# Kernel tuning notes

Measured on AMD Instinct MI355X. Metric: run time of the kernel, lower is better.

## Reference

```python
import jax, jax.numpy as jnp
import numpy as np

H = 32          # num_heads
DN = 128        # qk_nope_head_dim
DR = 64         # qk_rope_head_dim
DV = 128        # v_head_dim
HID = 4096      # hidden_size
QR = 1536       # q_lora_rank
KVR = 512       # kv_lora_rank
EPS = 1e-6
MAXP = 4096     # max_position_embeddings


def _rope_tables():
    inv_freq = 1.0 / (10000.0 ** (np.arange(0, DR, 2, dtype=np.float32) / DR))
    t = np.arange(MAXP, dtype=np.float32)
    freqs = np.outer(t, inv_freq)
    emb = np.concatenate([freqs, freqs], axis=-1)  # [MAXP, DR]
    return jnp.asarray(np.cos(emb), jnp.float32), jnp.asarray(np.sin(emb), jnp.float32)


def _rotate_half(x):
    x1, x2 = x[..., : x.shape[-1] // 2], x[..., x.shape[-1] // 2 :]
    return jnp.concatenate([-x2, x1], axis=-1)


def _rms_norm(x, w, eps=EPS):
    var = jnp.mean(jnp.square(x), axis=-1, keepdims=True)
    return x * jax.lax.rsqrt(var + eps) * w


def setup_inputs() -> dict:
    key = jax.random.key(0)
    ks = jax.random.split(key, 9)
    s = 0.02
    return {
        "hidden_states": jax.random.normal(ks[0], (2, 2048, HID), jnp.float32),
        "position_ids": jnp.arange(2 * 2048, dtype=jnp.int64).reshape(2, 2048) % MAXP,
        "q_a_w": jax.random.normal(ks[1], (QR, HID), jnp.float32) * s,
        "q_a_ln_w": jnp.ones((QR,), jnp.float32),
        "q_b_w": jax.random.normal(ks[2], (H * (DN + DR), QR), jnp.float32) * s,
        "kv_a_w": jax.random.normal(ks[3], (KVR, HID), jnp.float32) * s,
        "kv_a_ln_w": jnp.ones((KVR,), jnp.float32),
        "kv_b_w": jax.random.normal(ks[4], (H * (DN + DV), KVR), jnp.float32) * s,
        "k_rope_w": jax.random.normal(ks[5], (H * DR, HID), jnp.float32) * s,
        "o_w": jax.random.normal(ks[6], (HID, H * DV), jnp.float32) * s,
    }


def reference(hidden_states, position_ids, q_a_w, q_a_ln_w, q_b_w,
              kv_a_w, kv_a_ln_w, kv_b_w, k_rope_w, o_w):
    bsz, q_len, _ = hidden_states.shape
    cos_tab, sin_tab = _rope_tables()

    # Q low-rank path
    q = hidden_states @ q_a_w.T                      # [B,S,QR]
    q = _rms_norm(q, q_a_ln_w)
    q = q @ q_b_w.T                                  # [B,S,H*(DN+DR)]
    q = q.reshape(bsz, q_len, H, DN + DR).transpose(0, 2, 1, 3)  # [B,H,S,DN+DR]
    q_nope, q_rope = q[..., :DN], q[..., DN:]

    # KV low-rank path
    kv = _rms_norm(hidden_states @ kv_a_w.T, kv_a_ln_w)          # [B,S,KVR]
    kv = (kv @ kv_b_w.T).reshape(bsz, q_len, H, DN + DV).transpose(0, 2, 1, 3)
    k_nope, v = kv[..., :DN], kv[..., DN:]                        # [B,H,S,DN],[B,H,S,DV]

    k_rope = (hidden_states @ k_rope_w.T).reshape(bsz, q_len, H, DR).transpose(0, 2, 1, 3)

    # decoupled RoPE
    cos = cos_tab[position_ids][:, None, :, :]       # [B,1,S,DR]
    sin = sin_tab[position_ids][:, None, :, :]
    q_rope = q_rope * cos + _rotate_half(q_rope) * sin
    k_rope = k_rope * cos + _rotate_half(k_rope) * sin

    full_q = jnp.concatenate([q_nope, q_rope], axis=-1)  # [B,H,S,DN+DR]
    full_k = jnp.concatenate([k_nope, k_rope], axis=-1)

    scale = 1.0 / jnp.sqrt(jnp.float32(DN + DR))
    attn = jnp.einsum("bhqd,bhkd->bhqk", full_q, full_k) * scale
    attn = jax.nn.softmax(attn.astype(jnp.float32), axis=-1).astype(full_q.dtype)
    out = jnp.einsum("bhqk,bhkd->bhqd", attn, v)          # [B,H,S,DV]
    out = out.transpose(0, 2, 1, 3).reshape(bsz, q_len, H * DV)
    return out @ o_w.T                                     # [B,S,HID]
```

## Files before the change

kernel.cpp:

```cpp
#include <hip/hip_runtime.h>
#include <hip/hip_bf16.h>
#include <math.h>


typedef __attribute__((ext_vector_type(8))) short s16x8;
typedef __attribute__((ext_vector_type(4))) float f32x4;
typedef __attribute__((ext_vector_type(4))) unsigned short u16x4;

#define DEV __device__ __forceinline__

constexpr int Bc = 2, Sc = 2048, Tc = Bc * Sc;
constexpr int Hc = 32, DNc = 128, DRc = 64, DVc = 128;
constexpr int HIDc = 4096, QRc = 1536, KVRc = 512;
constexpr int DQK = DNc + DRc;

DEV unsigned short f2bf(float f) {
  unsigned u = __float_as_uint(f);
  return (unsigned short)((u + 0x7fffu + ((u >> 16) & 1u)) >> 16);
}
DEV float bf2f(unsigned short u) { return __uint_as_float(((unsigned)u) << 16); }

DEV void gll16(const void* g, void* l) {
  __builtin_amdgcn_global_load_lds((const __attribute__((address_space(1))) void*)g,
                                   (__attribute__((address_space(3))) void*)l, 16, 0, 0);
}
DEV f32x4 mfma_bf16(s16x8 a, s16x8 b, f32x4 c) {
  return __builtin_amdgcn_mfma_f32_16x16x32_bf16(a, b, c, 0, 0, 0);
}
DEV unsigned cvt_pk_bf16(float a, float b) {
  unsigned r;
  asm("v_cvt_pk_bf16_f32 %0, %1, %2" : "=v"(r) : "v"(a), "v"(b));
  return r;
}

__global__ __launch_bounds__(256) void cast_k(const float* __restrict__ in,
                                              unsigned short* __restrict__ out, long n) {
  long i = ((long)blockIdx.x * 256 + threadIdx.x) * 4;
  if (i >= n) return;
  float4 v = *(const float4*)(in + i);
  u16x4 o;
  o.x = f2bf(v.x); o.y = f2bf(v.y); o.z = f2bf(v.z); o.w = f2bf(v.w);
  *(u16x4*)(out + i) = o;
}

template <int COLS>
__global__ __launch_bounds__(256) void rmsnorm_bf_k(unsigned short* __restrict__ x,
                                                    const float* __restrict__ w,
                                                    int pitch) {
  const int row = blockIdx.x;
  unsigned short* p = x + (size_t)row * pitch;
  float ss = 0.f;
  for (int c = threadIdx.x * 8; c < COLS; c += 2048) {
    s16x8 v = *(const s16x8*)&p[c];
    #pragma unroll
    for (int j = 0; j < 8; ++j) { const float f = bf2f((unsigned short)v[j]); ss += f * f; }
  }
  #pragma unroll
  for (int off = 1; off < 64; off <<= 1) ss += __shfl_xor(ss, off, 64);
  __shared__ float sred[4];
  if ((threadIdx.x & 63) == 0) sred[threadIdx.x >> 6] = ss;
  __syncthreads();
  const float inv = rsqrtf((sred[0] + sred[1] + sred[2] + sred[3]) / (float)COLS + 1e-6f);
  for (int c = threadIdx.x * 8; c < COLS; c += 2048) {
    s16x8 v = *(const s16x8*)&p[c];
    s16x8 o;
    #pragma unroll
    for (int j = 0; j < 8; ++j)
      o[j] = (short)f2bf(bf2f((unsigned short)v[j]) * inv * w[c + j]);
    *(s16x8*)&p[c] = o;
  }
}

template <bool OUTF32>
__global__ __launch_bounds__(512, 2) void gemm256_bt(const unsigned short* __restrict__ A,
                                                     int lda,
                                                     const unsigned short* __restrict__ B,
                                                     void* __restrict__ Cout,
                                                     int M, int N, int K) {
  __shared__ unsigned short As[2][256 * 64];
  __shared__ unsigned short Bs[2][256 * 64];
  const int tid = threadIdx.x;
  const int wv = tid >> 6, l = tid & 63;
  const int lo = l & 15, hi = l >> 4;
  const int wm = wv >> 2, wn = wv & 3;
  const int nbx = N >> 8;
  const int nwg = (M >> 8) * nbx;
  const int orig = blockIdx.x;
  const int q8 = nwg >> 3, r8 = nwg & 7, xc = orig & 7, o8 = orig >> 3;
  const int wg = (xc < r8 ? xc * (q8 + 1) : r8 * (q8 + 1) + (xc - r8) * q8) + o8;
  const int bx = wg % nbx, by = wg / nbx;
  const int m0 = by * 256, n0 = bx * 256;
  const int lrow = l >> 3;
  const int lcol = (((l & 7) ^ lrow) << 3);

  f32x4 acc[8][4] = {};
  const int NKT = K >> 6;

  auto stage = [&](int bi, int kt) {
    #pragma unroll
    for (int i = 0; i < 4; ++i) {
      const int r0 = wv * 32 + i * 8;
      gll16(A + (size_t)(m0 + r0 + lrow) * lda + kt + lcol, (void*)&As[bi][r0 * 64]);
    }
    #pragma unroll
    for (int i = 0; i < 4; ++i) {
      const int r0 = wv * 32 + i * 8;
      gll16(B + (size_t)(n0 + r0 + lrow) * K + kt + lcol, (void*)&Bs[bi][r0 * 64]);
    }
  };

  stage(0, 0);

  for (int t = 0; t < NKT; ++t) {
    const int bi = t & 1;
    if (t + 1 < NKT) stage(bi ^ 1, (t + 1) * 64);
    __builtin_amdgcn_sched_barrier(0);
    if (t + 1 < NKT) asm volatile("s_waitcnt vmcnt(8)" ::: "memory");
    else             asm volatile("s_waitcnt vmcnt(0)" ::: "memory");
    __builtin_amdgcn_s_barrier();
    __builtin_amdgcn_sched_barrier(0);

    const unsigned short* Ab = As[bi];
    const unsigned short* Bb = Bs[bi];
    auto rdA = [&](int m, int kk) -> s16x8 {
      const int row = wm * 128 + m * 16 + lo;
      return *(const s16x8*)&Ab[row * 64 + ((kk * 32 + hi * 8) ^ ((row & 7) << 3))];
    };
    auto rdB = [&](int n, int kk) -> s16x8 {
      const int row = wn * 64 + n * 16 + lo;
      return *(const s16x8*)&Bb[row * 64 + ((kk * 32 + hi * 8) ^ ((row & 7) << 3))];
    };

    s16x8 a[4][2], b0[2][2], b2[2][2];
    #pragma unroll
    for (int m = 0; m < 4; ++m) { a[m][0] = rdA(m, 0); a[m][1] = rdA(m, 1); }
    #pragma unroll
    for (int n = 0; n < 2; ++n) { b0[n][0] = rdB(n, 0); b0[n][1] = rdB(n, 1); }
    __builtin_amdgcn_sched_barrier(0);
    __builtin_amdgcn_s_setprio(1);
    #pragma unroll
    for (int m = 0; m < 4; ++m)
      #pragma unroll
      for (int n = 0; n < 2; ++n) {
        acc[m][n] = mfma_bf16(a[m][0], b0[n][0], acc[m][n]);
        acc[m][n] = mfma_bf16(a[m][1], b0[n][1], acc[m][n]);
      }
    __builtin_amdgcn_s_setprio(0);
    __builtin_amdgcn_sched_barrier(0);
    __builtin_amdgcn_s_barrier();
    #pragma unroll
    for (int n = 0; n < 2; ++n) { b2[n][0] = rdB(n + 2, 0); b2[n][1] = rdB(n + 2, 1); }
    __builtin_amdgcn_sched_barrier(0);
    __builtin_amdgcn_s_setprio(1);
    #pragma unroll
    for (int m = 0; m < 4; ++m)
      #pragma unroll
      for (int n = 0; n < 2; ++n) {
        acc[m][n + 2] = mfma_bf16(a[m][0], b2[n][0], acc[m][n + 2]);
        acc[m][n + 2] = mfma_bf16(a[m][1], b2[n][1], acc[m][n + 2]);
      }
    __builtin_amdgcn_s_setprio(0);
    __builtin_amdgcn_sched_barrier(0);
    __builtin_amdgcn_s_barrier();
    #pragma unroll
    for (int m = 0; m < 4; ++m) { a[m][0] = rdA(m + 4, 0); a[m][1] = rdA(m + 4, 1); }
    __builtin_amdgcn_sched_barrier(0);
    __builtin_amdgcn_s_setprio(1);
    #pragma unroll
    for (int m = 0; m < 4; ++m)
      #pragma unroll
      for (int n = 0; n < 2; ++n) {
        acc[m + 4][n + 2] = mfma_bf16(a[m][0], b2[n][0], acc[m + 4][n + 2]);
        acc[m + 4][n + 2] = mfma_bf16(a[m][1], b2[n][1], acc[m + 4][n + 2]);
      }
    __builtin_amdgcn_s_setprio(0);
    __builtin_amdgcn_sched_barrier(0);
    __builtin_amdgcn_s_barrier();
    __builtin_amdgcn_s_setprio(1);
    #pragma unroll
    for (int m = 0; m < 4; ++m)
      #pragma unroll
      for (int n = 0; n < 2; ++n) {
        acc[m + 4][n] = mfma_bf16(a[m][0], b0[n][0], acc[m + 4][n]);
        acc[m + 4][n] = mfma_bf16(a[m][1], b0[n][1], acc[m + 4][n]);
      }
    __builtin_amdgcn_s_setprio(0);
    __builtin_amdgcn_sched_barrier(0);
    __builtin_amdgcn_s_barrier();
  }

  #pragma unroll
  for (int m = 0; m < 8; ++m)
    #pragma unroll
    for (int n = 0; n < 4; ++n)
      #pragma unroll
      for (int r = 0; r < 4; ++r) {
        const int row = m0 + wm * 128 + m * 16 + hi * 4 + r;
        const int col = n0 + wn * 64 + n * 16 + lo;
        const float v = acc[m][n][r];
        if (OUTF32) ((float*)Cout)[(size_t)row * N + col] = v;
        else ((unsigned short*)Cout)[(size_t)row * N + col] = f2bf(v);
      }
}

DEV void rope8(float pos, int j0, const s16x8& xv, const s16x8& pv, unsigned short* o) {
  #pragma unroll
  for (int j = 0; j < 8; ++j) {
    const int jj = j0 + j;
    const float inv = exp2f(-(float)(jj & 31) * 0.4152410118f);
    const float th = pos * inv;
    float sn, cs;
    sincosf(th, &sn, &cs);
    const float x = bf2f((unsigned short)xv[j]);
    const float pr = bf2f((unsigned short)pv[j]);
    const float rt = (jj < 32) ? -pr : pr;
    o[j] = f2bf(x * cs + rt * sn);
  }
}

__global__ __launch_bounds__(256) void rope_q_k(const unsigned short* __restrict__ qb,
                                                const int* __restrict__ pos,
                                                unsigned short* __restrict__ Qa) {
  const int gid = blockIdx.x * 256 + threadIdx.x;
  const int chunk = gid % 24, row = gid / 24;
  const int d0 = chunk * 8;
  const int bh = row >> 11, s = row & 2047;
  const int b = bh >> 5, h = bh & 31;
  const int token = b * 2048 + s;
  const unsigned short* src = qb + (size_t)token * (Hc * DQK) + h * DQK;
  unsigned short* dst = Qa + (size_t)row * DQK + d0;
  if (d0 < 128) { *(s16x8*)dst = *(const s16x8*)&src[d0]; return; }
  const int j0 = d0 - 128;
  s16x8 xv = *(const s16x8*)&src[128 + j0];
  s16x8 pv = *(const s16x8*)&src[128 + (j0 ^ 32)];
  unsigned short o[8];
  rope8((float)pos[token], j0, xv, pv, o);
  *(s16x8*)dst = *(const s16x8*)o;
}

__global__ __launch_bounds__(256) void rope_k_k(const unsigned short* __restrict__ kvb,
                                                const unsigned short* __restrict__ krb,
                                                const int* __restrict__ pos,
                                                unsigned short* __restrict__ Ka) {
  const int gid = blockIdx.x * 256 + threadIdx.x;
  const int chunk = gid % 24, row = gid / 24;
  const int d0 = chunk * 8;
  const int bh = row >> 11, s = row & 2047;
  const int b = bh >> 5, h = bh & 31;
  const int token = b * 2048 + s;
  unsigned short* dst = Ka + (size_t)row * DQK + d0;
  if (d0 < 128) {
    *(s16x8*)dst = *(const s16x8*)(kvb + (size_t)token * (Hc * 256) + h * 256 + d0);
    return;
  }
  const int j0 = d0 - 128;
  const unsigned short* src = krb + (size_t)token * HIDc + h * DRc;
  s16x8 xv = *(const s16x8*)&src[j0];
  s16x8 pv = *(const s16x8*)&src[j0 ^ 32];
  unsigned short o[8];
  rope8((float)pos[token], j0, xv, pv, o);
  *(s16x8*)dst = *(const s16x8*)o;
}

__global__ __launch_bounds__(512, 2) void attn_k(const unsigned short* __restrict__ Q,
                                                 const unsigned short* __restrict__ Kt,
                                                 const unsigned short* __restrict__ KV,
                                                 unsigned short* __restrict__ O) {
  __shared__ unsigned short Ks[2][64 * 192];
  __shared__ unsigned short Vs[2][128 * 64];
  __shared__ unsigned short Ps[8][32 * 64];
  const int bh = blockIdx.x, qblk = blockIdx.y;
  const int b = bh >> 5, h = bh & 31;
  const int tid = threadIdx.x, w = tid >> 6, l = tid & 63;
  const int lo = l & 15, hi = l >> 4;
  const int sw = (lo & 7) << 3;
  const unsigned short* Qb = Q + (size_t)bh * Sc * DQK;
  const unsigned short* Kb = Kt + (size_t)bh * Sc * DQK;
  const int qrow0 = qblk * 256 + w * 32;
  const float c2 = 0.10411759f;

  s16x8 qfr[2][6];
  #pragma unroll
  for (int qf = 0; qf < 2; ++qf)
    #pragma unroll
    for (int dc = 0; dc < 6; ++dc)
      qfr[qf][dc] = *(const s16x8*)&Qb[(size_t)(qrow0 + qf * 16 + lo) * DQK + dc * 32 + hi * 8];

  f32x4 oacc[2][8] = {};
  float mrow[2] = {-INFINITY, -INFINITY};
  float lrow[2] = {0.f, 0.f};

  s16x8 vv[2];
  auto stageK = [&](int kb, int kt) {
    #pragma unroll
    for (int i = 0; i < 3; ++i) {
      const int o = (w * 3 + i) * 1024 + l * 16;
      const int rr = o / 384, cc = o % 384;
      const int scc = cc ^ ((rr & 7) << 4);
      gll16(Kb + (size_t)(kt + rr) * DQK + (scc >> 1), (void*)&Ks[kb][(w * 3 + i) * 512]);
    }
  };
  auto loadV = [&](int kt) {
    #pragma unroll
    for (int it = 0; it < 2; ++it) {
      const int dv0 = (w * 2 + it) * 8;
      vv[it] = *(const s16x8*)(KV + (size_t)(b * Sc + kt + l) * (Hc * 256) + h * 256 + 128 + dv0);
    }
  };
  auto writeV = [&](int vb) {
    #pragma unroll
    for (int it = 0; it < 2; ++it) {
      const int dv0 = (w * 2 + it) * 8;
      #pragma unroll
      for (int j = 0; j < 8; ++j) {
        const int dv = dv0 + j;
        Vs[vb][(dv * 64 + l) ^ ((dv & 7) << 3)] = (unsigned short)vv[it][j];
      }
    }
  };

  constexpr int NT = Sc / 64;
  loadV(0);
  stageK(0, 0);
  writeV(0);
  asm volatile("s_waitcnt vmcnt(0) lgkmcnt(0)" ::: "memory");
  __builtin_amdgcn_s_barrier();
  __builtin_amdgcn_sched_barrier(0);
  int cur = 0;

  for (int t = 0; t < NT; ++t) {
    const bool pre = (t + 1 < NT);
    if (pre) {
      loadV((t + 1) * 64);
      __builtin_amdgcn_sched_barrier(0);
      stageK(cur ^ 1, (t + 1) * 64);
      __builtin_amdgcn_sched_barrier(0);
    }

    f32x4 sc[2][4] = {};
    #pragma unroll
    for (int cf = 0; cf < 4; ++cf) {
      const int krow = cf * 16 + lo;
      #pragma unroll
      for (int dc = 0; dc < 6; ++dc) {
        s16x8 kf = *(const s16x8*)&Ks[cur][(krow * 192 + dc * 32 + hi * 8) ^ ((krow & 7) << 3)];
        sc[0][cf] = mfma_bf16(kf, qfr[0][dc], sc[0][cf]);
        sc[1][cf] = mfma_bf16(kf, qfr[1][dc], sc[1][cf]);
      }
    }

    #pragma unroll
    for (int qf = 0; qf < 2; ++qf) {
      float mx = sc[qf][0][0];
      #pragma unroll
      for (int cf = 0; cf < 4; ++cf)
        #pragma unroll
        for (int r = 0; r < 4; ++r) mx = fmaxf(mx, sc[qf][cf][r]);
      mx = fmaxf(mx, __shfl_xor(mx, 16, 64));
      mx = fmaxf(mx, __shfl_xor(mx, 32, 64));
      const float nm = fmaxf(mrow[qf], mx * c2);
      const float alpha = exp2f(mrow[qf] - nm);
      mrow[qf] = nm;
      float psum = 0.f;
      const int qrow = qf * 16 + lo;
      #pragma unroll
      for (int cf = 0; cf < 4; ++cf) {
        float p0 = exp2f(fmaf(sc[qf][cf][0], c2, -nm));
        float p1 = exp2f(fmaf(sc[qf][cf][1], c2, -nm));
        float p2 = exp2f(fmaf(sc[qf][cf][2], c2, -nm));
        float p3 = exp2f(fmaf(sc[qf][cf][3], c2, -nm));
        psum += (p0 + p1) + (p2 + p3);
        const int ka = cf * 16 + hi * 4;
        *(unsigned*)&Ps[w][qrow * 64 + ((ka + 0) ^ sw)] = cvt_pk_bf16(p0, p1);
        *(unsigned*)&Ps[w][qrow * 64 + ((ka + 2) ^ sw)] = cvt_pk_bf16(p2, p3);
      }
      psum += __shfl_xor(psum, 16, 64);
      psum += __shfl_xor(psum, 32, 64);
      lrow[qf] = lrow[qf] * alpha + psum;
      #pragma unroll
      for (int r = 0; r < 4; ++r) {
        const float ar = __shfl(alpha, hi * 4 + r, 64);
        #pragma unroll
        for (int dvf = 0; dvf < 8; ++dvf) oacc[qf][dvf][r] *= ar;
      }
    }

    #pragma unroll
    for (int hf = 0; hf < 2; ++hf) {
      s16x8 pa0 = *(const s16x8*)&Ps[w][lo * 64 + ((hf * 32 + hi * 8) ^ sw)];
      s16x8 pa1 = *(const s16x8*)&Ps[w][(16 + lo) * 64 + ((hf * 32 + hi * 8) ^ sw)];
      #pragma unroll
      for (int dvf = 0; dvf < 8; ++dvf) {
        const int dv = dvf * 16 + lo;
        s16x8 vb = *(const s16x8*)&Vs[cur][(dv * 64 + hf * 32 + hi * 8) ^ ((dv & 7) << 3)];
        oacc[0][dvf] = mfma_bf16(pa0, vb, oacc[0][dvf]);
        oacc[1][dvf] = mfma_bf16(pa1, vb, oacc[1][dvf]);
      }
    }

    if (pre) writeV(cur ^ 1);
    asm volatile("s_waitcnt vmcnt(0) lgkmcnt(0)" ::: "memory");
    __builtin_amdgcn_s_barrier();
    __builtin_amdgcn_sched_barrier(0);
    cur ^= 1;
  }

  #pragma unroll
  for (int qf = 0; qf < 2; ++qf)
    #pragma unroll
    for (int r = 0; r < 4; ++r) {
      const float linv = 1.f / __shfl(lrow[qf], hi * 4 + r, 64);
      const int q = qrow0 + qf * 16 + hi * 4 + r;
      #pragma unroll
      for (int dvf = 0; dvf < 8; ++dvf)
        O[(size_t)(b * Sc + q) * (Hc * DVc) + h * DVc + dvf * 16 + lo] =
            f2bf(oacc[qf][dvf][r] * linv);
    }
}

extern "C" void kernel_launch(void* const* d_in, const int* in_sizes, int n_in,
                              void* d_out, int out_size, void* d_ws, size_t ws_size,
                              hipStream_t stream) {
  const float* hs      = (const float*)d_in[0];
  const int*   posids  = (const int*)d_in[1];
  const float* qa_w    = (const float*)d_in[2];
  const float* qa_ln   = (const float*)d_in[3];
  const float* qb_w    = (const float*)d_in[4];
  const float* kva_w   = (const float*)d_in[5];
  const float* kva_ln  = (const float*)d_in[6];
  const float* kvb_w   = (const float*)d_in[7];
  const float* kr_w    = (const float*)d_in[8];
  const float* o_w     = (const float*)d_in[9];
  float* out = (float*)d_out;

  char* ws = (char*)d_ws;
  const size_t offF = 0;
  const size_t offR = offF + 33554432;
  const size_t offD = offR + 35651584;
  const size_t offA = offD + 50331648;
  const size_t offB = offA + 67108864;

  unsigned short* hs_bf  = (unsigned short*)(ws + offF);
  unsigned short* w_qb   = (unsigned short*)(ws + offF);
  unsigned short* w_kvb  = (unsigned short*)(ws + offF);
  unsigned short* attn_o = (unsigned short*)(ws + offF);
  unsigned short* cbuf   = (unsigned short*)(ws + offR);
  unsigned short* q_buf  = (unsigned short*)(ws + offD);
  unsigned short* Ka     = (unsigned short*)(ws + offD);
  unsigned short* kv_buf = (unsigned short*)(ws + offA);
  unsigned short* cw     = (unsigned short*)(ws + offB);
  unsigned short* Qa     = (unsigned short*)(ws + offB);
  unsigned short* w_o    = (unsigned short*)(ws + offB);

  auto cast = [&](const float* src, unsigned short* dst, long n) {
    cast_k<<<dim3((unsigned)((n / 4 + 255) / 256)), dim3(256), 0, stream>>>(src, dst, n);
  };
  auto g256_bf = [&](const unsigned short* A, int lda, const unsigned short* B,
                     unsigned short* C, int M, int N, int K) {
    gemm256_bt<false><<<dim3((M / 256) * (N / 256)), dim3(512), 0, stream>>>(A, lda, B, (void*)C, M, N, K);
  };
  auto g256_f32 = [&](const unsigned short* A, int lda, const unsigned short* B,
                      float* C, int M, int N, int K) {
    gemm256_bt<true><<<dim3((M / 256) * (N / 256)), dim3(512), 0, stream>>>(A, lda, B, (void*)C, M, N, K);
  };

  cast(hs, hs_bf, (long)Tc * HIDc);

  cast(qa_w,  cw,                              (long)QRc * HIDc);
  cast(kva_w, cw + (size_t)QRc * HIDc,         (long)KVRc * HIDc);
  cast(kr_w,  cw + (size_t)(QRc + KVRc) * HIDc,(long)Hc * DRc * HIDc);

  g256_bf(hs_bf, HIDc, cw, cbuf, Tc, HIDc, HIDc);

  rmsnorm_bf_k<QRc><<<dim3(Tc), dim3(256), 0, stream>>>(cbuf, qa_ln, HIDc);
  rmsnorm_bf_k<KVRc><<<dim3(Tc), dim3(256), 0, stream>>>(cbuf + QRc, kva_ln, HIDc);

  cast(qb_w, w_qb, (long)Hc * DQK * QRc);
  g256_bf(cbuf, HIDc, w_qb, q_buf, Tc, Hc * DQK, QRc);

  cast(kvb_w, w_kvb, (long)Hc * 256 * KVRc);
  g256_bf(cbuf + QRc, HIDc, w_kvb, kv_buf, Tc, Hc * 256, KVRc);

  const int nchunks = Bc * Hc * Sc * 24;
  rope_q_k<<<dim3(nchunks / 256), dim3(256), 0, stream>>>(q_buf, posids, Qa);
  rope_k_k<<<dim3(nchunks / 256), dim3(256), 0, stream>>>(kv_buf, cbuf + QRc + KVRc, posids, Ka);

  attn_k<<<dim3(Bc * Hc, Sc / 256), dim3(512), 0, stream>>>(Qa, Ka, kv_buf, attn_o);

  cast(o_w, w_o, (long)HIDc * Hc * DVc);
  g256_f32(attn_o, Hc * DVc, w_o, out, Tc, HIDc, Hc * DVc);

  (void)in_sizes; (void)n_in; (void)out_size; (void)ws_size;
}
```

Baseline: 877.6 us.

## Single-buffer V, shrink P scratch, lazy softmax rescale to raise attention occupancy

Replaces the double-buffered V tile with a single buffer and an extra barrier before the refill. Halves the per-warp P scratch by writing and consuming P in two 32-column halves. Skips the running-max rescale of the accumulators unless the max grows by more than 8 in log2 units. Together these cut LDS use so four blocks per CU can be requested. The cost is an extra barrier per iteration, less overlap of V loads with compute, and register pressure from the tighter launch bound.

```diff
diff --git a/kernel.cpp b/kernel.cpp
--- a/kernel.cpp
+++ b/kernel.cpp
@@ -262,18 +262,18 @@
   *(s16x8*)dst = *(const s16x8*)o;
 }
 
-__global__ __launch_bounds__(512, 2) void attn_k(const unsigned short* __restrict__ Q,
+__global__ __launch_bounds__(512, 4) void attn_k(const unsigned short* __restrict__ Q,
                                                  const unsigned short* __restrict__ Kt,
                                                  const unsigned short* __restrict__ KV,
                                                  unsigned short* __restrict__ O) {
   __shared__ unsigned short Ks[2][64 * 192];
-  __shared__ unsigned short Vs[2][128 * 64];
-  __shared__ unsigned short Ps[8][32 * 64];
+  __shared__ unsigned short Vs[128 * 64];
+  __shared__ unsigned short Ps[8][32 * 32];
   const int bh = blockIdx.x, qblk = blockIdx.y;
   const int b = bh >> 5, h = bh & 31;
   const int tid = threadIdx.x, w = tid >> 6, l = tid & 63;
   const int lo = l & 15, hi = l >> 4;
-  const int sw = (lo & 7) << 3;
+  const int sw2 = (lo & 3) << 3;
   const unsigned short* Qb = Q + (size_t)bh * Sc * DQK;
   const unsigned short* Kb = Kt + (size_t)bh * Sc * DQK;
   const int qrow0 = qblk * 256 + w * 32;
@@ -307,14 +307,14 @@
       vv[it] = *(const s16x8*)(KV + (size_t)(b * Sc + kt + l) * (Hc * 256) + h * 256 + 128 + dv0);
     }
   };
-  auto writeV = [&](int vb) {
+  auto writeV = [&]() {
     #pragma unroll
     for (int it = 0; it < 2; ++it) {
       const int dv0 = (w * 2 + it) * 8;
       #pragma unroll
       for (int j = 0; j < 8; ++j) {
         const int dv = dv0 + j;
-        Vs[vb][(dv * 64 + l) ^ ((dv & 7) << 3)] = (unsigned short)vv[it][j];
+        Vs[(dv * 64 + l) ^ ((dv & 7) << 3)] = (unsigned short)vv[it][j];
       }
     }
   };
@@ -322,8 +322,9 @@
   constexpr int NT = Sc / 64;
   loadV(0);
   stageK(0, 0);
-  writeV(0);
-  asm volatile("s_waitcnt vmcnt(0) lgkmcnt(0)" ::: "memory");
+  asm volatile("s_waitcnt vmcnt(0)" ::: "memory");
+  writeV();
+  asm volatile("s_waitcnt lgkmcnt(0)" ::: "memory");
   __builtin_amdgcn_s_barrier();
   __builtin_amdgcn_sched_barrier(0);
   int cur = 0;
@@ -358,48 +359,61 @@
         for (int r = 0; r < 4; ++r) mx = fmaxf(mx, sc[qf][cf][r]);
       mx = fmaxf(mx, __shfl_xor(mx, 16, 64));
       mx = fmaxf(mx, __shfl_xor(mx, 32, 64));
-      const float nm = fmaxf(mrow[qf], mx * c2);
-      const float alpha = exp2f(mrow[qf] - nm);
-      mrow[qf] = nm;
+      const float mxl = mx * c2;
+      if (!__all(mxl - mrow[qf] <= 8.f)) {
+        const float nm = fmaxf(mrow[qf], mxl);
+        const float alpha = exp2f(mrow[qf] - nm);
+        mrow[qf] = nm;
+        lrow[qf] *= alpha;
+        #pragma unroll
+        for (int r = 0; r < 4; ++r) {
+          const float ar = __shfl(alpha, hi * 4 + r, 64);
+          #pragma unroll
+          for (int dvf = 0; dvf < 8; ++dvf) oacc[qf][dvf][r] *= ar;
+        }
+      }
       float psum = 0.f;
-      const int qrow = qf * 16 + lo;
       #pragma unroll
       for (int cf = 0; cf < 4; ++cf) {
-        float p0 = exp2f(fmaf(sc[qf][cf][0], c2, -nm));
-        float p1 = exp2f(fmaf(sc[qf][cf][1], c2, -nm));
-        float p2 = exp2f(fmaf(sc[qf][cf][2], c2, -nm));
-        float p3 = exp2f(fmaf(sc[qf][cf][3], c2, -nm));
-        psum += (p0 + p1) + (p2 + p3);
-        const int ka = cf * 16 + hi * 4;
-        *(unsigned*)&Ps[w][qrow * 64 + ((ka + 0) ^ sw)] = cvt_pk_bf16(p0, p1);
-        *(unsigned*)&Ps[w][qrow * 64 + ((ka + 2) ^ sw)] = cvt_pk_bf16(p2, p3);
+        sc[qf][cf][0] = exp2f(fmaf(sc[qf][cf][0], c2, -mrow[qf]));
+        sc[qf][cf][1] = exp2f(fmaf(sc[qf][cf][1], c2, -mrow[qf]));
+        sc[qf][cf][2] = exp2f(fmaf(sc[qf][cf][2], c2, -mrow[qf]));
+        sc[qf][cf][3] = exp2f(fmaf(sc[qf][cf][3], c2, -mrow[qf]));
+        psum += (sc[qf][cf][0] + sc[qf][cf][1]) + (sc[qf][cf][2] + sc[qf][cf][3]);
       }
       psum += __shfl_xor(psum, 16, 64);
       psum += __shfl_xor(psum, 32, 64);
-      lrow[qf] = lrow[qf] * alpha + psum;
-      #pragma unroll
-      for (int r = 0; r < 4; ++r) {
-        const float ar = __shfl(alpha, hi * 4 + r, 64);
+      lrow[qf] += psum;
+    }
+
+    #pragma unroll
+    for (int hf = 0; hf < 2; ++hf) {
+      #pragma unroll
+      for (int qf = 0; qf < 2; ++qf) {
+        const int qrow = qf * 16 + lo;
         #pragma unroll
-        for (int dvf = 0; dvf < 8; ++dvf) oacc[qf][dvf][r] *= ar;
-      }
-    }
-
-    #pragma unroll
-    for (int hf = 0; hf < 2; ++hf) {
-      s16x8 pa0 = *(const s16x8*)&Ps[w][lo * 64 + ((hf * 32 + hi * 8) ^ sw)];
-      s16x8 pa1 = *(const s16x8*)&Ps[w][(16 + lo) * 64 + ((hf * 32 + hi * 8) ^ sw)];
+        for (int ci = 0; ci < 2; ++ci) {
+          const int cf = 2 * hf + ci;
+          const int ka = ci * 16 + hi * 4;
+          *(unsigned*)&Ps[w][qrow * 32 + ((ka + 0) ^ sw2)] = cvt_pk_bf16(sc[qf][cf][0], sc[qf][cf][1]);
+          *(unsigned*)&Ps[w][qrow * 32 + ((ka + 2) ^ sw2)] = cvt_pk_bf16(sc[qf][cf][2], sc[qf][cf][3]);
+        }
+      }
+      s16x8 pa0 = *(const s16x8*)&Ps[w][lo * 32 + ((hi * 8) ^ sw2)];
+      s16x8 pa1 = *(const s16x8*)&Ps[w][(16 + lo) * 32 + ((hi * 8) ^ sw2)];
       #pragma unroll
       for (int dvf = 0; dvf < 8; ++dvf) {
         const int dv = dvf * 16 + lo;
-        s16x8 vb = *(const s16x8*)&Vs[cur][(dv * 64 + hf * 32 + hi * 8) ^ ((dv & 7) << 3)];
+        s16x8 vb = *(const s16x8*)&Vs[(dv * 64 + hf * 32 + hi * 8) ^ ((dv & 7) << 3)];
         oacc[0][dvf] = mfma_bf16(pa0, vb, oacc[0][dvf]);
         oacc[1][dvf] = mfma_bf16(pa1, vb, oacc[1][dvf]);
       }
     }
 
-    if (pre) writeV(cur ^ 1);
-    asm volatile("s_waitcnt vmcnt(0) lgkmcnt(0)" ::: "memory");
+    asm volatile("s_waitcnt vmcnt(0)" ::: "memory");
+    __builtin_amdgcn_s_barrier();
+    if (pre) writeV();
+    asm volatile("s_waitcnt lgkmcnt(0)" ::: "memory");
     __builtin_amdgcn_s_barrier();
     __builtin_amdgcn_sched_barrier(0);
     cur ^= 1;
```

Result: slower. 1.860 ms (+111.9%).

## Write GEMM outputs directly in head-major layout and apply RoPE in place

Applied to the files above, without the earlier changes.

The q_b and kv_b GEMM epilogues now scatter results straight into the per-head Q/K attention layouts, with V split into a compact buffer. This removes the separate copy of the nope parts in the rope kernels. The rope kernels now only touch the 64 rope dims, using paired rotate-half math that handles both halves in one thread. The trade-off is more index arithmetic and scattered stores in the GEMM epilogue.

```diff
diff --git a/kernel.cpp b/kernel.cpp
--- a/kernel.cpp
+++ b/kernel.cpp
@@ -71,11 +71,12 @@
   }
 }
 
-template <bool OUTF32>
+template <int MODE>
 __global__ __launch_bounds__(512, 2) void gemm256_bt(const unsigned short* __restrict__ A,
                                                      int lda,
                                                      const unsigned short* __restrict__ B,
                                                      void* __restrict__ Cout,
+                                                     void* __restrict__ Cout2,
                                                      int M, int N, int K) {
   __shared__ unsigned short As[2][256 * 64];
   __shared__ unsigned short Bs[2][256 * 64];
@@ -198,68 +199,73 @@
         const int row = m0 + wm * 128 + m * 16 + hi * 4 + r;
         const int col = n0 + wn * 64 + n * 16 + lo;
         const float v = acc[m][n][r];
-        if (OUTF32) ((float*)Cout)[(size_t)row * N + col] = v;
-        else ((unsigned short*)Cout)[(size_t)row * N + col] = f2bf(v);
-      }
-}
-
-DEV void rope8(float pos, int j0, const s16x8& xv, const s16x8& pv, unsigned short* o) {
+        if (MODE == 1) {
+          ((float*)Cout)[(size_t)row * N + col] = v;
+        } else if (MODE == 0) {
+          ((unsigned short*)Cout)[(size_t)row * N + col] = f2bf(v);
+        } else if (MODE == 2) {
+          const int hh = col / DQK, dd = col % DQK;
+          const int bb = row >> 11, ss = row & 2047;
+          ((unsigned short*)Cout)[((size_t)((bb * Hc + hh) * Sc + ss)) * DQK + dd] = f2bf(v);
+        } else {
+          const int hh = col >> 8, cc = col & 255;
+          const int bb = row >> 11, ss = row & 2047;
+          if (cc < 128)
+            ((unsigned short*)Cout)[((size_t)((bb * Hc + hh) * Sc + ss)) * DQK + cc] = f2bf(v);
+          else
+            ((unsigned short*)Cout2)[(size_t)row * (Hc * DVc) + hh * DVc + (cc - 128)] = f2bf(v);
+        }
+      }
+}
+
+DEV void rope_pair8(float pos, int j0, const s16x8& x1, const s16x8& x2,
+                    s16x8& o1, s16x8& o2) {
   #pragma unroll
   for (int j = 0; j < 8; ++j) {
     const int jj = j0 + j;
-    const float inv = exp2f(-(float)(jj & 31) * 0.4152410118f);
-    const float th = pos * inv;
+    const float inv = exp2f(-(float)jj * 0.4152410118f);
     float sn, cs;
-    sincosf(th, &sn, &cs);
-    const float x = bf2f((unsigned short)xv[j]);
-    const float pr = bf2f((unsigned short)pv[j]);
-    const float rt = (jj < 32) ? -pr : pr;
-    o[j] = f2bf(x * cs + rt * sn);
+    sincosf(pos * inv, &sn, &cs);
+    const float a = bf2f((unsigned short)x1[j]);
+    const float c = bf2f((unsigned short)x2[j]);
+    o1[j] = f2bf(a * cs - c * sn);
+    o2[j] = f2bf(c * cs + a * sn);
   }
 }
 
-__global__ __launch_bounds__(256) void rope_q_k(const unsigned short* __restrict__ qb,
-                                                const int* __restrict__ pos,
-                                                unsigned short* __restrict__ Qa) {
+__global__ __launch_bounds__(256) void rope_q_k(unsigned short* __restrict__ Qa,
+                                                const int* __restrict__ pos) {
   const int gid = blockIdx.x * 256 + threadIdx.x;
-  const int chunk = gid % 24, row = gid / 24;
-  const int d0 = chunk * 8;
-  const int bh = row >> 11, s = row & 2047;
-  const int b = bh >> 5, h = bh & 31;
-  const int token = b * 2048 + s;
-  const unsigned short* src = qb + (size_t)token * (Hc * DQK) + h * DQK;
-  unsigned short* dst = Qa + (size_t)row * DQK + d0;
-  if (d0 < 128) { *(s16x8*)dst = *(const s16x8*)&src[d0]; return; }
-  const int j0 = d0 - 128;
-  s16x8 xv = *(const s16x8*)&src[128 + j0];
-  s16x8 pv = *(const s16x8*)&src[128 + (j0 ^ 32)];
-  unsigned short o[8];
-  rope8((float)pos[token], j0, xv, pv, o);
-  *(s16x8*)dst = *(const s16x8*)o;
-}
-
-__global__ __launch_bounds__(256) void rope_k_k(const unsigned short* __restrict__ kvb,
-                                                const unsigned short* __restrict__ krb,
-                                                const int* __restrict__ pos,
-                                                unsigned short* __restrict__ Ka) {
+  const int pr = gid & 3, rowp = gid >> 2;
+  const int j0 = pr * 8;
+  const int bh = rowp >> 11, s = rowp & 2047;
+  const int token = (bh >> 5) * Sc + s;
+  unsigned short* base = Qa + (size_t)rowp * DQK + 128;
+  s16x8 x1 = *(const s16x8*)&base[j0];
+  s16x8 x2 = *(const s16x8*)&base[j0 + 32];
+  s16x8 o1, o2;
+  rope_pair8((float)pos[token], j0, x1, x2, o1, o2);
+  *(s16x8*)&base[j0] = o1;
+  *(s16x8*)&base[j0 + 32] = o2;
+}
+
+__global__ __launch_bounds__(256) void rope_k2_k(const unsigned short* __restrict__ kr,
+                                                 const int* __restrict__ pos,
+                                                 unsigned short* __restrict__ Ka) {
   const int gid = blockIdx.x * 256 + threadIdx.x;
-  const int chunk = gid % 24, row = gid / 24;
-  const int d0 = chunk * 8;
-  const int bh = row >> 11, s = row & 2047;
-  const int b = bh >> 5, h = bh & 31;
-  const int token = b * 2048 + s;
-  unsigned short* dst = Ka + (size_t)row * DQK + d0;
-  if (d0 < 128) {
-    *(s16x8*)dst = *(const s16x8*)(kvb + (size_t)token * (Hc * 256) + h * 256 + d0);
-    return;
-  }
-  const int j0 = d0 - 128;
-  const unsigned short* src = krb + (size_t)token * HIDc + h * DRc;
-  s16x8 xv = *(const s16x8*)&src[j0];
-  s16x8 pv = *(const s16x8*)&src[j0 ^ 32];
-  unsigned short o[8];
-  rope8((float)pos[token], j0, xv, pv, o);
-  *(s16x8*)dst = *(const s16x8*)o;
+  const int pr = gid & 3, rowp = gid >> 2;
+  const int j0 = pr * 8;
+  const int bh = rowp >> 11, s = rowp & 2047;
+  const int h = bh & 31;
+  const int token = (bh >> 5) * Sc + s;
+  const unsigned short* src = kr + (size_t)token * HIDc + h * DRc;
+  s16x8 x1 = *(const s16x8*)&src[j0];
+  s16x8 x2 = *(const s16x8*)&src[j0 + 32];
+  s16x8 o1, o2;
+  rope_pair8((float)pos[token], j0, x1, x2, o1, o2);
+  unsigned short* dst = Ka + (size_t)rowp * DQK + 128;
+  *(s16x8*)&dst[j0] = o1;
+  *(s16x8*)&dst[j0 + 32] = o2;
 }
 
 __global__ __launch_bounds__(512, 2) void attn_k(const unsigned short* __restrict__ Q,
@@ -304,7 +310,7 @@
     #pragma unroll
     for (int it = 0; it < 2; ++it) {
       const int dv0 = (w * 2 + it) * 8;
-      vv[it] = *(const s16x8*)(KV + (size_t)(b * Sc + kt + l) * (Hc * 256) + h * 256 + 128 + dv0);
+      vv[it] = *(const s16x8*)(KV + (size_t)(b * Sc + kt + l) * (Hc * DVc) + h * DVc + dv0);
     }
   };
   auto writeV = [&](int vb) {
@@ -445,9 +451,8 @@
   unsigned short* w_kvb  = (unsigned short*)(ws + offF);
   unsigned short* attn_o = (unsigned short*)(ws + offF);
   unsigned short* cbuf   = (unsigned short*)(ws + offR);
-  unsigned short* q_buf  = (unsigned short*)(ws + offD);
   unsigned short* Ka     = (unsigned short*)(ws + offD);
-  unsigned short* kv_buf = (unsigned short*)(ws + offA);
+  unsigned short* kv_v   = (unsigned short*)(ws + offA);
   unsigned short* cw     = (unsigned short*)(ws + offB);
   unsigned short* Qa     = (unsigned short*)(ws + offB);
   unsigned short* w_o    = (unsigned short*)(ws + offB);
@@ -455,14 +460,6 @@
   auto cast = [&](const float* src, unsigned short* dst, long n) {
     cast_k<<<dim3((unsigned)((n / 4 + 255) / 256)), dim3(256), 0, stream>>>(src, dst, n);
   };
-  auto g256_bf = [&](const unsigned short* A, int lda, const unsigned short* B,
-                     unsigned short* C, int M, int N, int K) {
-    gemm256_bt<false><<<dim3((M / 256) * (N / 256)), dim3(512), 0, stream>>>(A, lda, B, (void*)C, M, N, K);
-  };
-  auto g256_f32 = [&](const unsigned short* A, int lda, const unsigned short* B,
-                      float* C, int M, int N, int K) {
-    gemm256_bt<true><<<dim3((M / 256) * (N / 256)), dim3(512), 0, stream>>>(A, lda, B, (void*)C, M, N, K);
-  };
 
   cast(hs, hs_bf, (long)Tc * HIDc);
 
@@ -470,25 +467,33 @@
   cast(kva_w, cw + (size_t)QRc * HIDc,         (long)KVRc * HIDc);
   cast(kr_w,  cw + (size_t)(QRc + KVRc) * HIDc,(long)Hc * DRc * HIDc);
 
-  g256_bf(hs_bf, HIDc, cw, cbuf, Tc, HIDc, HIDc);
+  gemm256_bt<0><<<dim3(16 * 16), dim3(512), 0, stream>>>(hs_bf, HIDc, cw,
+                                                         (void*)cbuf, nullptr,
+                                                         Tc, HIDc, HIDc);
 
   rmsnorm_bf_k<QRc><<<dim3(Tc), dim3(256), 0, stream>>>(cbuf, qa_ln, HIDc);
   rmsnorm_bf_k<KVRc><<<dim3(Tc), dim3(256), 0, stream>>>(cbuf + QRc, kva_ln, HIDc);
 
   cast(qb_w, w_qb, (long)Hc * DQK * QRc);
-  g256_bf(cbuf, HIDc, w_qb, q_buf, Tc, Hc * DQK, QRc);
+  gemm256_bt<2><<<dim3(16 * 24), dim3(512), 0, stream>>>(cbuf, HIDc, w_qb,
+                                                         (void*)Qa, nullptr,
+                                                         Tc, Hc * DQK, QRc);
 
   cast(kvb_w, w_kvb, (long)Hc * 256 * KVRc);
-  g256_bf(cbuf + QRc, HIDc, w_kvb, kv_buf, Tc, Hc * 256, KVRc);
-
-  const int nchunks = Bc * Hc * Sc * 24;
-  rope_q_k<<<dim3(nchunks / 256), dim3(256), 0, stream>>>(q_buf, posids, Qa);
-  rope_k_k<<<dim3(nchunks / 256), dim3(256), 0, stream>>>(kv_buf, cbuf + QRc + KVRc, posids, Ka);
-
-  attn_k<<<dim3(Bc * Hc, Sc / 256), dim3(512), 0, stream>>>(Qa, Ka, kv_buf, attn_o);
+  gemm256_bt<3><<<dim3(16 * 32), dim3(512), 0, stream>>>(cbuf + QRc, HIDc, w_kvb,
+                                                         (void*)Ka, (void*)kv_v,
+                                                         Tc, Hc * 256, KVRc);
+
+  const int npair = Bc * Hc * Sc * 4;
+  rope_q_k<<<dim3(npair / 256), dim3(256), 0, stream>>>(Qa, posids);
+  rope_k2_k<<<dim3(npair / 256), dim3(256), 0, stream>>>(cbuf + QRc + KVRc, posids, Ka);
+
+  attn_k<<<dim3(Bc * Hc, Sc / 256), dim3(512), 0, stream>>>(Qa, Ka, kv_v, attn_o);
 
   cast(o_w, w_o, (long)HIDc * Hc * DVc);
-  g256_f32(attn_o, Hc * DVc, w_o, out, Tc, HIDc, Hc * DVc);
+  gemm256_bt<1><<<dim3(16 * 16), dim3(512), 0, stream>>>(attn_o, Hc * DVc, w_o,
+                                                         (void*)out, nullptr,
+                                                         Tc, HIDc, Hc * DVc);
 
   (void)in_sizes; (void)n_in; (void)out_size; (void)ws_size;
 }
```

After: 841.2 us. 1.04x faster.
